# Performance work log

Measured on AMD Instinct MI355X. Metric: run time of the kernel, lower is better.

The kernel has to match this reference:

```python
import jax, jax.numpy as jnp
import numpy as np

NHEAD = 8

def setup_inputs() -> dict:
    key = jax.random.key(0)
    ks = jax.random.split(key, 6)
    b, n, d = 4, 1024, 512
    emb = jax.random.normal(ks[0], (b, n, d), dtype=jnp.float32)
    dirs = jax.random.normal(ks[1], (b, n, n, 3), dtype=jnp.float32)
    d_mask = jax.random.normal(ks[2], (b * NHEAD, n, n), dtype=jnp.float32) * 0.1
    W_proj = jax.random.normal(ks[3], (d, 3 * d), dtype=jnp.float32) / np.sqrt(d)
    b_proj = jnp.zeros((3 * d,), dtype=jnp.float32)
    w_force = jax.random.normal(ks[4], (d,), dtype=jnp.float32) / np.sqrt(d)
    b_force = jnp.zeros((1,), dtype=jnp.float32)
    return {"emb": emb, "dirs": dirs, "d_mask": d_mask, "W_proj": W_proj,
            "b_proj": b_proj, "w_force": w_force, "b_force": b_force}

def reference(emb, dirs, d_mask, W_proj, b_proj, w_force, b_force):
    b, n, d = emb.shape
    h = NHEAD
    dh = d // h
    scale = jnp.asarray(np.sqrt(d), emb.dtype)
    qkv = emb @ W_proj + b_proj                      # (b,n,3d)
    q, k, v = jnp.split(qkv, 3, axis=-1)
    q = q.reshape(b, n, h, dh).transpose(0, 2, 1, 3) / scale   # (b,h,n,dh)
    k = k.reshape(b, n, h, dh).transpose(0, 2, 1, 3)           # (b,h,n,dh)
    v = v.reshape(b, n, h, dh).transpose(0, 2, 1, 3)           # (b,h,n,dh)
    scores = jnp.einsum('bhid,bhjd->bhij', q, k) + d_mask.reshape(b, h, n, n)
    attn = jax.nn.softmax(scores, axis=-1)                     # (b,h,n,n); dropout in eval mode = identity
    # torch: (attn[...,None] * dirs[:,None]) @ v  materializes (b,h,n,n,3);
    # fused einsum computes the same per-axis weighted sum without it.
    xyz = jnp.einsum('bhij,bija,bhjd->biahd', attn, dirs, v)   # (b,n,3,h,dh)
    xyz = xyz.reshape(b, n, 3, d)
    out = jnp.einsum('bnad,d->bna', xyz, w_force) + b_force[0]  # (b,n,3)
    return out
```

## Files before the change

kernel.cpp:

```cpp
#include <hip/hip_runtime.h>
#include <hip/hip_bf16.h>

#define NH 8
#define BB 4
#define NN 1024
#define DD 512
#define DH 64

typedef __bf16 bf16x8 __attribute__((ext_vector_type(8)));
typedef float f32x4 __attribute__((ext_vector_type(4)));

__device__ __forceinline__ unsigned short f2bf(float f) {
    union { float f; unsigned u; } v; v.f = f;
    unsigned u = v.u;
    unsigned r = u + 0x7FFFu + ((u >> 16) & 1u);
    return (unsigned short)(r >> 16);
}
__device__ __forceinline__ float b2f(unsigned short u) {
    union { unsigned u; float f; } cv; cv.u = ((unsigned)u) << 16; return cv.f;
}

__global__ __launch_bounds__(256) void k_prep(const float* __restrict__ W,
                                              const float* __restrict__ b_proj,
                                              const float* __restrict__ w_force,
                                              unsigned short* __restrict__ Wt,
                                              float* __restrict__ bias_eff,
                                              float* __restrict__ wv_eff,
                                              float* __restrict__ s_bias) {
    __shared__ float tile[32][33];
    int bx = blockIdx.x;
    int t = threadIdx.x;
    const float rscale = 0.044194173824159216f;
    if (bx < 512) {
        int c0 = (bx & 15) * 32;
        int n0 = (bx >> 4) * 32;
        for (int i = 0; i < 4; ++i) {
            int idx = t + i * 256;
            int r = idx >> 5, cn = idx & 31;
            tile[r][cn] = W[(c0 + r) * (3 * DD) + n0 + cn];
        }
        __syncthreads();
        for (int i = 0; i < 4; ++i) {
            int idx = t + i * 256;
            int nn = idx >> 5, cc = idx & 31;
            float v = tile[cc][nn];
            int n = n0 + nn;
            if (n < DD) v *= rscale;
            Wt[n * DD + c0 + cc] = f2bf(v);
        }
        if ((bx & 15) == 0 && t < 32) {
            int n = n0 + t;
            bias_eff[n] = b_proj[n] * (n < DD ? rscale : 1.0f);
        }
        return;
    }
    int wave = t >> 6, lane = t & 63;
    if (bx == 640) {
        if (wave == 0) {
            for (int hh = 0; hh < NH; ++hh) {
                float p = b_proj[2 * DD + hh * DH + lane] * w_force[hh * DH + lane];
                for (int off = 32; off; off >>= 1) p += __shfl_xor(p, off);
                if (lane == 0) s_bias[hh] = p;
            }
        }
        return;
    }
    int c = (bx - 512) * 4 + wave;
    const float* wr = W + (size_t)c * (3 * DD) + 2 * DD;
    #pragma unroll
    for (int hh = 0; hh < NH; ++hh) {
        float p = wr[hh * DH + lane] * w_force[hh * DH + lane];
        for (int off = 32; off; off >>= 1) p += __shfl_xor(p, off);
        if (lane == 0) wv_eff[c * 8 + hh] = p;
    }
}

__global__ __launch_bounds__(128) void k_s(const float* __restrict__ emb,
                                           const float* __restrict__ wv_eff,
                                           const float* __restrict__ s_bias,
                                           float* __restrict__ s_ws) {
    int t = blockIdx.x * 128 + threadIdx.x;
    int row = t >> 3;
    int h = t & 7;
    const float* er = emb + (size_t)row * DD;
    const float* wp = wv_eff + h;
    float acc = 0.f;
    #pragma unroll 8
    for (int c4 = 0; c4 < DD / 4; ++c4) {
        float4 e = *(const float4*)(er + c4 * 4);
        acc += e.x * wp[(c4 * 4 + 0) * 8];
        acc += e.y * wp[(c4 * 4 + 1) * 8];
        acc += e.z * wp[(c4 * 4 + 2) * 8];
        acc += e.w * wp[(c4 * 4 + 3) * 8];
    }
    int b = row >> 10, j = row & 1023;
    s_ws[(b * 8 + h) * NN + j] = acc + s_bias[h];
}

__global__ __launch_bounds__(256) void k_gemm(const float* __restrict__ emb,
                                              const unsigned short* __restrict__ Wt,
                                              const float* __restrict__ bias_eff,
                                              unsigned short* __restrict__ qb,
                                              unsigned short* __restrict__ kb) {
    __shared__ __align__(16) unsigned short a_s[128 * 32];
    __shared__ __align__(16) unsigned short b_s[128 * 32];
    int m0 = blockIdx.x * 128, n0 = blockIdx.y * 128;
    int t = threadIdx.x;
    int wave = t >> 6, lane = t & 63;
    int wr = (wave >> 1) * 64, wc = (wave & 1) * 64;
    int qd = lane >> 4, c = lane & 15;
    int sr = t >> 2, sg = (t & 3) * 8;
    f32x4 acc[4][4] = {};
    for (int k0 = 0; k0 < DD; k0 += 32) {
        float4 x0 = *(const float4*)(emb + (size_t)(m0 + sr) * DD + k0 + sg);
        float4 x1 = *(const float4*)(emb + (size_t)(m0 + sr) * DD + k0 + sg + 4);
        float4 y0 = *(const float4*)(emb + (size_t)(m0 + 64 + sr) * DD + k0 + sg);
        float4 y1 = *(const float4*)(emb + (size_t)(m0 + 64 + sr) * DD + k0 + sg + 4);
        uint4 bv0 = *(const uint4*)(Wt + (size_t)(n0 + sr) * DD + k0 + sg);
        uint4 bv1 = *(const uint4*)(Wt + (size_t)(n0 + 64 + sr) * DD + k0 + sg);
        union { unsigned short u[8]; uint4 v; } px, py;
        px.u[0] = f2bf(x0.x); px.u[1] = f2bf(x0.y); px.u[2] = f2bf(x0.z); px.u[3] = f2bf(x0.w);
        px.u[4] = f2bf(x1.x); px.u[5] = f2bf(x1.y); px.u[6] = f2bf(x1.z); px.u[7] = f2bf(x1.w);
        py.u[0] = f2bf(y0.x); py.u[1] = f2bf(y0.y); py.u[2] = f2bf(y0.z); py.u[3] = f2bf(y0.w);
        py.u[4] = f2bf(y1.x); py.u[5] = f2bf(y1.y); py.u[6] = f2bf(y1.z); py.u[7] = f2bf(y1.w);
        __syncthreads();
        *(uint4*)(&a_s[sr * 32 + sg]) = px.v;
        *(uint4*)(&a_s[(64 + sr) * 32 + sg]) = py.v;
        *(uint4*)(&b_s[sr * 32 + sg]) = bv0;
        *(uint4*)(&b_s[(64 + sr) * 32 + sg]) = bv1;
        __syncthreads();
        bf16x8 af[4], bfr[4];
        #pragma unroll
        for (int mi = 0; mi < 4; ++mi)
            af[mi] = *(const bf16x8*)(&a_s[(wr + mi * 16 + c) * 32 + qd * 8]);
        #pragma unroll
        for (int ni = 0; ni < 4; ++ni)
            bfr[ni] = *(const bf16x8*)(&b_s[(wc + ni * 16 + c) * 32 + qd * 8]);
        #pragma unroll
        for (int mi = 0; mi < 4; ++mi)
            #pragma unroll
            for (int ni = 0; ni < 4; ++ni)
                acc[mi][ni] = __builtin_amdgcn_mfma_f32_16x16x32_bf16(af[mi], bfr[ni], acc[mi][ni], 0, 0, 0);
    }
    bool isQ = (n0 < DD);
    unsigned short* dst = isQ ? qb : kb;
    int nb = isQ ? n0 : n0 - DD;
    #pragma unroll
    for (int mi = 0; mi < 4; ++mi)
        #pragma unroll
        for (int ni = 0; ni < 4; ++ni) {
            int col = nb + wc + ni * 16 + c;
            float be = bias_eff[isQ ? col : col + DD];
            #pragma unroll
            for (int r = 0; r < 4; ++r) {
                int row = m0 + wr + mi * 16 + qd * 4 + r;
                dst[(size_t)row * DD + col] = f2bf(acc[mi][ni][r] + be);
            }
        }
}

__global__ __launch_bounds__(256) void k_qk(const unsigned short* __restrict__ qb,
                                            const unsigned short* __restrict__ kb,
                                            unsigned short* __restrict__ sc,
                                            int b0) {
    int bx = blockIdx.x;
    int bp = bx >> 7;
    int h = (bx >> 4) & 7;
    int itile = bx & 15;
    int i0 = itile * 64;
    int b = b0 + bp;
    int t = threadIdx.x;
    int w = t >> 6, lane = t & 63, qd = lane >> 4, c = lane & 15;

    bf16x8 aq0[4], aq1[4];
    #pragma unroll
    for (int s = 0; s < 4; ++s) {
        const unsigned short* qbase =
            qb + ((size_t)(b * NN + i0 + s * 16 + c) * DD + h * DH + qd * 8);
        aq0[s] = *(const bf16x8*)(qbase);
        aq1[s] = *(const bf16x8*)(qbase + 32);
    }
    unsigned short* scb = sc + ((size_t)(bp * NH + h)) * NN * NN;
    int j0w = w * 256;
    #pragma unroll
    for (int jt = 0; jt < 16; ++jt) {
        int j0 = j0w + jt * 16;
        const unsigned short* kba =
            kb + ((size_t)(b * NN + j0 + c) * DD + h * DH + qd * 8);
        bf16x8 kf0 = *(const bf16x8*)(kba);
        bf16x8 kf1 = *(const bf16x8*)(kba + 32);
        #pragma unroll
        for (int s = 0; s < 4; ++s) {
            f32x4 a = {0.f, 0.f, 0.f, 0.f};
            a = __builtin_amdgcn_mfma_f32_16x16x32_bf16(kf0, aq0[s], a, 0, 0, 0);
            a = __builtin_amdgcn_mfma_f32_16x16x32_bf16(kf1, aq1[s], a, 0, 0, 0);
            ushort4 pk;
            pk.x = f2bf(a[0]); pk.y = f2bf(a[1]); pk.z = f2bf(a[2]); pk.w = f2bf(a[3]);
            *(ushort4*)(scb + (size_t)(i0 + s * 16 + c) * NN + j0 + qd * 4) = pk;
        }
    }
}

__global__ __launch_bounds__(512, 4) void k_soft(const unsigned short* __restrict__ sc,
                                                 const float* __restrict__ s_ws,
                                                 const float* __restrict__ d_mask,
                                                 const float* __restrict__ dirs,
                                                 float* __restrict__ part,
                                                 int b0) {
    int bx = blockIdx.x;
    int bp = bx >> 10;
    int i = bx & 1023;
    int b = b0 + bp;
    int t = threadIdx.x;
    int h = t >> 6, lane = t & 63;
    int bh = b * NH + h;

    const float* sm = s_ws + (size_t)bh * NN;
    float4 sv[4];
    #pragma unroll
    for (int seg = 0; seg < 4; ++seg)
        sv[seg] = *(const float4*)(sm + seg * 256 + lane * 4);

    const float* mrow = d_mask + ((size_t)bh * NN + i) * NN + lane * 4;
    const float* drow = dirs + ((size_t)(b * NN + i) * NN + (size_t)(lane * 4)) * 3;
    const unsigned short* scrow = sc + ((size_t)(bp * NH + h) * NN + i) * NN + lane * 4;

    float l = 0.f, a0 = 0.f, a1 = 0.f, a2 = 0.f;
    #pragma unroll
    for (int seg = 0; seg < 4; ++seg) {
        float4 mk = *(const float4*)(mrow + seg * 256);
        float4 d0 = *(const float4*)(drow + seg * 768);
        float4 d1 = *(const float4*)(drow + seg * 768 + 4);
        float4 d2 = *(const float4*)(drow + seg * 768 + 8);
        ushort4 scv = *(const ushort4*)(scrow + seg * 256);
        float p0 = __expf(b2f(scv.x) + mk.x);
        float p1 = __expf(b2f(scv.y) + mk.y);
        float p2 = __expf(b2f(scv.z) + mk.z);
        float p3 = __expf(b2f(scv.w) + mk.w);
        l += p0 + p1 + p2 + p3;
        float t0 = p0 * sv[seg].x, t1 = p1 * sv[seg].y;
        float t2 = p2 * sv[seg].z, t3 = p3 * sv[seg].w;
        a0 += t0 * d0.x + t1 * d0.w + t2 * d1.z + t3 * d2.y;
        a1 += t0 * d0.y + t1 * d1.x + t2 * d1.w + t3 * d2.z;
        a2 += t0 * d0.z + t1 * d1.y + t2 * d2.x + t3 * d2.w;
    }

    #pragma unroll
    for (int off = 1; off < 64; off <<= 1) {
        l  += __shfl_xor(l, off);
        a0 += __shfl_xor(a0, off);
        a1 += __shfl_xor(a1, off);
        a2 += __shfl_xor(a2, off);
    }
    if (lane == 0) {
        f32x4 o; o[0] = l; o[1] = a0; o[2] = a1; o[3] = a2;
        *(f32x4*)(part + ((size_t)bh * NN + i) * 4) = o;
    }
}

__global__ __launch_bounds__(256) void k_fin(const float4* __restrict__ part,
                                             const float* __restrict__ b_force,
                                             float* __restrict__ out) {
    int t = blockIdx.x * 256 + threadIdx.x;
    int b = t >> 10, i = t & 1023;
    float o0, o1, o2;
    o0 = o1 = o2 = b_force[0];
    #pragma unroll
    for (int h = 0; h < NH; ++h) {
        float4 p = part[(((size_t)(b * NH + h)) << 10) + i];
        float inv = 1.0f / p.x;
        o0 += p.y * inv; o1 += p.z * inv; o2 += p.w * inv;
    }
    out[t * 3 + 0] = o0;
    out[t * 3 + 1] = o1;
    out[t * 3 + 2] = o2;
}

extern "C" void kernel_launch(void* const* d_in, const int* in_sizes, int n_in,
                              void* d_out, int out_size, void* d_ws, size_t ws_size,
                              hipStream_t stream) {
    (void)in_sizes; (void)n_in; (void)out_size; (void)ws_size;
    const float* emb     = (const float*)d_in[0];
    const float* dirs    = (const float*)d_in[1];
    const float* d_mask  = (const float*)d_in[2];
    const float* W       = (const float*)d_in[3];
    const float* b_proj  = (const float*)d_in[4];
    const float* w_force = (const float*)d_in[5];
    const float* b_force = (const float*)d_in[6];
    float* out = (float*)d_out;

    char* ws = (char*)d_ws;
    float* wv_eff   = (float*)ws;
    float* s_bias   = wv_eff + 4096;
    float* bias_eff = s_bias + 8;
    float* s_ws     = bias_eff + 1024;
    unsigned short* Wt = (unsigned short*)(s_ws + 32768);
    unsigned short* qb = Wt + 1024 * 512;
    unsigned short* kb = qb + 4096 * 512;
    float* part = (float*)(kb + 4096 * 512);
    unsigned short* scg = (unsigned short*)(part + 32 * 1024 * 4);

    hipLaunchKernelGGL(k_prep, dim3(641),      dim3(256), 0, stream,
                       W, b_proj, w_force, Wt, bias_eff, wv_eff, s_bias);
    hipLaunchKernelGGL(k_s,    dim3(256),      dim3(128), 0, stream, emb, wv_eff, s_bias, s_ws);
    hipLaunchKernelGGL(k_gemm, dim3(32, 8),    dim3(256), 0, stream, emb, Wt, bias_eff, qb, kb);
    for (int pair = 0; pair < 2; ++pair) {
        hipLaunchKernelGGL(k_qk,   dim3(256),  dim3(256), 0, stream, qb, kb, scg, pair * 2);
        hipLaunchKernelGGL(k_soft, dim3(2048), dim3(512), 0, stream,
                           scg, s_ws, d_mask, dirs, part, pair * 2);
    }
    hipLaunchKernelGGL(k_fin,  dim3(16),       dim3(256), 0, stream, (const float4*)part, b_force, out);
}
```

Baseline: 324.8 us.

## Pre-convert emb to bf16 and run QK/softmax over all batches at once

```diff
diff --git a/kernel.cpp b/kernel.cpp
--- a/kernel.cpp
+++ b/kernel.cpp
@@ -78,7 +78,8 @@
 __global__ __launch_bounds__(128) void k_s(const float* __restrict__ emb,
                                            const float* __restrict__ wv_eff,
                                            const float* __restrict__ s_bias,
-                                           float* __restrict__ s_ws) {
+                                           float* __restrict__ s_ws,
+                                           unsigned short* __restrict__ embb) {
     int t = blockIdx.x * 128 + threadIdx.x;
     int row = t >> 3;
     int h = t & 7;
@@ -95,9 +96,17 @@
     }
     int b = row >> 10, j = row & 1023;
     s_ws[(b * 8 + h) * NN + j] = acc + s_bias[h];
-}
-
-__global__ __launch_bounds__(256) void k_gemm(const float* __restrict__ emb,
+    unsigned short* eb = embb + (size_t)row * DD + h * 64;
+    #pragma unroll
+    for (int k = 0; k < 16; ++k) {
+        float4 e = *(const float4*)(er + h * 64 + k * 4);
+        ushort4 pk;
+        pk.x = f2bf(e.x); pk.y = f2bf(e.y); pk.z = f2bf(e.z); pk.w = f2bf(e.w);
+        *(ushort4*)(eb + k * 4) = pk;
+    }
+}
+
+__global__ __launch_bounds__(256) void k_gemm(const unsigned short* __restrict__ embb,
                                               const unsigned short* __restrict__ Wt,
                                               const float* __restrict__ bias_eff,
                                               unsigned short* __restrict__ qb,
@@ -112,20 +121,13 @@
     int sr = t >> 2, sg = (t & 3) * 8;
     f32x4 acc[4][4] = {};
     for (int k0 = 0; k0 < DD; k0 += 32) {
-        float4 x0 = *(const float4*)(emb + (size_t)(m0 + sr) * DD + k0 + sg);
-        float4 x1 = *(const float4*)(emb + (size_t)(m0 + sr) * DD + k0 + sg + 4);
-        float4 y0 = *(const float4*)(emb + (size_t)(m0 + 64 + sr) * DD + k0 + sg);
-        float4 y1 = *(const float4*)(emb + (size_t)(m0 + 64 + sr) * DD + k0 + sg + 4);
+        uint4 av0 = *(const uint4*)(embb + (size_t)(m0 + sr) * DD + k0 + sg);
+        uint4 av1 = *(const uint4*)(embb + (size_t)(m0 + 64 + sr) * DD + k0 + sg);
         uint4 bv0 = *(const uint4*)(Wt + (size_t)(n0 + sr) * DD + k0 + sg);
         uint4 bv1 = *(const uint4*)(Wt + (size_t)(n0 + 64 + sr) * DD + k0 + sg);
-        union { unsigned short u[8]; uint4 v; } px, py;
-        px.u[0] = f2bf(x0.x); px.u[1] = f2bf(x0.y); px.u[2] = f2bf(x0.z); px.u[3] = f2bf(x0.w);
-        px.u[4] = f2bf(x1.x); px.u[5] = f2bf(x1.y); px.u[6] = f2bf(x1.z); px.u[7] = f2bf(x1.w);
-        py.u[0] = f2bf(y0.x); py.u[1] = f2bf(y0.y); py.u[2] = f2bf(y0.z); py.u[3] = f2bf(y0.w);
-        py.u[4] = f2bf(y1.x); py.u[5] = f2bf(y1.y); py.u[6] = f2bf(y1.z); py.u[7] = f2bf(y1.w);
         __syncthreads();
-        *(uint4*)(&a_s[sr * 32 + sg]) = px.v;
-        *(uint4*)(&a_s[(64 + sr) * 32 + sg]) = py.v;
+        *(uint4*)(&a_s[sr * 32 + sg]) = av0;
+        *(uint4*)(&a_s[(64 + sr) * 32 + sg]) = av1;
         *(uint4*)(&b_s[sr * 32 + sg]) = bv0;
         *(uint4*)(&b_s[(64 + sr) * 32 + sg]) = bv1;
         __syncthreads();
@@ -161,14 +163,12 @@
 
 __global__ __launch_bounds__(256) void k_qk(const unsigned short* __restrict__ qb,
                                             const unsigned short* __restrict__ kb,
-                                            unsigned short* __restrict__ sc,
-                                            int b0) {
+                                            unsigned short* __restrict__ sc) {
     int bx = blockIdx.x;
-    int bp = bx >> 7;
+    int b = bx >> 7;
     int h = (bx >> 4) & 7;
     int itile = bx & 15;
     int i0 = itile * 64;
-    int b = b0 + bp;
     int t = threadIdx.x;
     int w = t >> 6, lane = t & 63, qd = lane >> 4, c = lane & 15;
 
@@ -180,7 +180,7 @@
         aq0[s] = *(const bf16x8*)(qbase);
         aq1[s] = *(const bf16x8*)(qbase + 32);
     }
-    unsigned short* scb = sc + ((size_t)(bp * NH + h)) * NN * NN;
+    unsigned short* scb = sc + ((size_t)(b * NH + h)) * NN * NN;
     int j0w = w * 256;
     #pragma unroll
     for (int jt = 0; jt < 16; ++jt) {
@@ -205,12 +205,10 @@
                                                  const float* __restrict__ s_ws,
                                                  const float* __restrict__ d_mask,
                                                  const float* __restrict__ dirs,
-                                                 float* __restrict__ part,
-                                                 int b0) {
+                                                 float* __restrict__ part) {
     int bx = blockIdx.x;
-    int bp = bx >> 10;
+    int b = bx >> 10;
     int i = bx & 1023;
-    int b = b0 + bp;
     int t = threadIdx.x;
     int h = t >> 6, lane = t & 63;
     int bh = b * NH + h;
@@ -223,7 +221,7 @@
 
     const float* mrow = d_mask + ((size_t)bh * NN + i) * NN + lane * 4;
     const float* drow = dirs + ((size_t)(b * NN + i) * NN + (size_t)(lane * 4)) * 3;
-    const unsigned short* scrow = sc + ((size_t)(bp * NH + h) * NN + i) * NN + lane * 4;
+    const unsigned short* scrow = sc + ((size_t)bh * NN + i) * NN + lane * 4;
 
     float l = 0.f, a0 = 0.f, a1 = 0.f, a2 = 0.f;
     #pragma unroll
@@ -298,16 +296,17 @@
     unsigned short* qb = Wt + 1024 * 512;
     unsigned short* kb = qb + 4096 * 512;
     float* part = (float*)(kb + 4096 * 512);
-    unsigned short* scg = (unsigned short*)(part + 32 * 1024 * 4);
+    unsigned short* scg  = (unsigned short*)(part + 32 * 1024 * 4);
+    unsigned short* embb = scg + (size_t)BB * NH * NN * NN;
 
     hipLaunchKernelGGL(k_prep, dim3(641),      dim3(256), 0, stream,
                        W, b_proj, w_force, Wt, bias_eff, wv_eff, s_bias);
-    hipLaunchKernelGGL(k_s,    dim3(256),      dim3(128), 0, stream, emb, wv_eff, s_bias, s_ws);
-    hipLaunchKernelGGL(k_gemm, dim3(32, 8),    dim3(256), 0, stream, emb, Wt, bias_eff, qb, kb);
-    for (int pair = 0; pair < 2; ++pair) {
-        hipLaunchKernelGGL(k_qk,   dim3(256),  dim3(256), 0, stream, qb, kb, scg, pair * 2);
-        hipLaunchKernelGGL(k_soft, dim3(2048), dim3(512), 0, stream,
-                           scg, s_ws, d_mask, dirs, part, pair * 2);
-    }
+    hipLaunchKernelGGL(k_s,    dim3(256),      dim3(128), 0, stream,
+                       emb, wv_eff, s_bias, s_ws, embb);
+    hipLaunchKernelGGL(k_gemm, dim3(32, 8),    dim3(256), 0, stream,
+                       embb, Wt, bias_eff, qb, kb);
+    hipLaunchKernelGGL(k_qk,   dim3(512),      dim3(256), 0, stream, qb, kb, scg);
+    hipLaunchKernelGGL(k_soft, dim3(4096),     dim3(512), 0, stream,
+                       scg, s_ws, d_mask, dirs, part);
     hipLaunchKernelGGL(k_fin,  dim3(16),       dim3(256), 0, stream, (const float4*)part, b_force, out);
 }
```

Result: slower. 363.9 us (+12.0%).
